# Optimization experiments

Hardware: AMD Instinct MI355X
Metric: run time of the kernel (lower is better)

The kernel has to match this reference:

```python
import jax, jax.numpy as jnp
import numpy as np

N_NODES = 20000
N_EDGES = 320000
EMB = 256
K_DIFF = 3
BN_EPS = 1e-5


def conv1d(x, w, b, stride):
    # x: [N, Cin, L], w: [Cout, Cin, K]
    y = jax.lax.conv_general_dilated(x, w, window_strides=(stride,), padding='VALID',
                                     dimension_numbers=('NCH', 'OIH', 'NCH'))
    return y + b[None, :, None]


def batchnorm_train(x, gamma, beta):
    # training-mode BatchNorm1d over (N, L) per channel, biased variance
    m = jnp.mean(x, axis=(0, 2), keepdims=True)
    v = jnp.var(x, axis=(0, 2), keepdims=True)
    return (x - m) * jax.lax.rsqrt(v + BN_EPS) * gamma[None, :, None] + beta[None, :, None]


def dconv(X, W, b, row, col, norm_out, norm_in, n):
    # Diffusion convolution (pytorch_geometric_temporal DConv), K hops,
    # forward (out-degree) and backward (in-degree) random walks.
    def prop(x, norm):
        msg = norm[:, None] * x[row]                    # [E, F] gather
        return jax.ops.segment_sum(msg, col, num_segments=n)  # scatter-add to targets

    K = W.shape[1]
    Tx_0 = X
    Tx_1 = X
    H = X @ W[0, 0] + X @ W[1, 0]
    if K > 1:
        Tx_1_o = prop(X, norm_out)
        Tx_1_i = prop(X, norm_in)
        H = H + Tx_1_o @ W[0, 1] + Tx_1_i @ W[1, 1]
    for k in range(2, K):
        Tx_2_o = 2.0 * prop(Tx_1_o, norm_out) - Tx_0
        Tx_2_i = 2.0 * prop(Tx_1_i, norm_in) - Tx_0
        H = H + Tx_2_o @ W[0, k] + Tx_2_i @ W[1, k]
        Tx_0, Tx_1_o, Tx_1_i = Tx_1, Tx_2_o, Tx_2_i
    return H + b


def setup_inputs() -> dict:
    key = jax.random.key(0)
    ks = jax.random.split(key, 16)
    d_in = 2 * EMB  # concat([X, H])
    inp = {
        'x': jax.random.normal(ks[0], (N_NODES, 1, 100), dtype=jnp.float32),
        'edge_index': jax.random.randint(ks[1], (2, N_EDGES), 0, N_NODES, dtype=jnp.int32),
        'hidden_state': jax.random.normal(ks[2], (N_NODES, EMB), dtype=jnp.float32),
        'conv1_w': jax.random.normal(ks[3], (32, 1, 10), dtype=jnp.float32) * 0.2,
        'conv1_b': jnp.zeros((32,), jnp.float32),
        'bn1_gamma': jnp.ones((32,), jnp.float32),
        'bn1_beta': jnp.zeros((32,), jnp.float32),
        'conv2_w': jax.random.normal(ks[4], (32, 32, 10), dtype=jnp.float32) * 0.05,
        'conv2_b': jnp.zeros((32,), jnp.float32),
        'bn2_gamma': jnp.ones((32,), jnp.float32),
        'bn2_beta': jnp.zeros((32,), jnp.float32),
        'W_z': jax.random.normal(ks[5], (2, K_DIFF, d_in, EMB), dtype=jnp.float32) * 0.05,
        'b_z': jnp.zeros((EMB,), jnp.float32),
        'W_r': jax.random.normal(ks[6], (2, K_DIFF, d_in, EMB), dtype=jnp.float32) * 0.05,
        'b_r': jnp.zeros((EMB,), jnp.float32),
        'W_h': jax.random.normal(ks[7], (2, K_DIFF, d_in, EMB), dtype=jnp.float32) * 0.05,
        'b_h': jnp.zeros((EMB,), jnp.float32),
    }
    return inp


def reference(x, edge_index, hidden_state, conv1_w, conv1_b, bn1_gamma, bn1_beta,
              conv2_w, conv2_b, bn2_gamma, bn2_beta, W_z, b_z, W_r, b_r, W_h, b_h):
    n = x.shape[0]
    # CNN embedding: conv -> relu -> bn, twice
    h = batchnorm_train(jax.nn.relu(conv1d(x, conv1_w, conv1_b, 3)), bn1_gamma, bn1_beta)
    h = batchnorm_train(jax.nn.relu(conv1d(h, conv2_w, conv2_b, 3)), bn2_gamma, bn2_beta)
    X = h.reshape(n, -1)  # [N, EMB]

    row, col = edge_index[0], edge_index[1]
    ones = jnp.ones((row.shape[0],), X.dtype)
    deg_out = jax.ops.segment_sum(ones, row, num_segments=n)
    deg_in = jax.ops.segment_sum(ones, col, num_segments=n)
    norm_out = (1.0 / deg_out)[row]
    norm_in = (1.0 / deg_in)[col]

    H0 = hidden_state
    XH = jnp.concatenate([X, H0], axis=1)
    Z = jax.nn.sigmoid(dconv(XH, W_z, b_z, row, col, norm_out, norm_in, n))
    R = jax.nn.sigmoid(dconv(XH, W_r, b_r, row, col, norm_out, norm_in, n))
    XRH = jnp.concatenate([X, R * H0], axis=1)
    H_tilde = jnp.tanh(dconv(XRH, W_h, b_h, row, col, norm_out, norm_in, n))
    H = Z * H0 + (1.0 - Z) * H_tilde
    return jax.nn.relu(H)
```

## Files before the change

### kernel.cpp

```cpp
#include <hip/hip_runtime.h>
#include <cstdint>
#include <cstddef>

#define NN 20000
#define NE 320000

typedef float f32x4 __attribute__((ext_vector_type(4)));
typedef short s16x8 __attribute__((ext_vector_type(8)));

struct KB10 { const unsigned short* p[10]; };
struct PPB { const unsigned short* yo0; const unsigned short* yo1;
             const unsigned short* yi0; const unsigned short* yi1;
             unsigned short* po0; unsigned short* po1;
             unsigned short* pi0; unsigned short* pi1; };

__device__ __forceinline__ unsigned short f2bf(float x){
    unsigned u = __float_as_uint(x);
    unsigned r = (u + 0x7fffu + ((u >> 16) & 1u)) >> 16;
    return (unsigned short)r;
}
__device__ __forceinline__ float bf2f(unsigned short s){
    return __uint_as_float(((unsigned)s) << 16);
}

__device__ __forceinline__ void gl16(const void* g, void* l){
    __builtin_amdgcn_global_load_lds((const __attribute__((address_space(1))) unsigned int*)g,
                                     (__attribute__((address_space(3))) unsigned int*)l, 16, 0, 0);
}


__global__ void k_zero(uint32_t* p, int n){
    int i = blockIdx.x*256 + threadIdx.x;
    if(i < n) p[i] = 0u;
}

__global__ void k_degree(const int* __restrict__ ei, int* degout, int* degin){
    int e = blockIdx.x*256 + threadIdx.x;
    if(e < NE){
        atomicAdd(&degout[ei[e]], 1);
        atomicAdd(&degin[ei[NE+e]], 1);
    }
}

__global__ void k_scan(const int* __restrict__ degin, int* __restrict__ coloff,
                       float* __restrict__ invdegin){
    __shared__ int part[1024];
    int t = threadIdx.x;
    int base = t*20;
    int s = 0;
    for(int k=0;k<20;k++){ int i = base+k; if(i < NN) s += degin[i]; }
    part[t] = s;
    __syncthreads();
    for(int off=1; off<1024; off<<=1){
        int v = (t>=off) ? part[t-off] : 0;
        __syncthreads();
        part[t] += v;
        __syncthreads();
    }
    int run = (t>0) ? part[t-1] : 0;
    for(int k=0;k<20;k++){
        int i = base+k;
        if(i < NN){
            int d = degin[i];
            coloff[i] = run;
            run += d;
            invdegin[i] = (d>0) ? (1.0f/(float)d) : 0.0f;
        }
    }
    if(t==1023) coloff[NN] = part[1023];
}

__global__ void k_csr(const int* __restrict__ ei, const int* __restrict__ degout,
                      const int* __restrict__ coloff, int* cnt,
                      int* __restrict__ esrc, float* __restrict__ enormo){
    int e = blockIdx.x*256 + threadIdx.x;
    if(e < NE){
        int r = ei[e], c = ei[NE+e];
        int pos = coloff[c] + atomicAdd(&cnt[c], 1);
        esrc[pos] = r;
        enormo[pos] = 1.0f/(float)degout[r];
    }
}


__global__ void k_conv1(const float* __restrict__ x, const float* __restrict__ w1,
                        const float* __restrict__ b1, unsigned short* __restrict__ y1b){
    __shared__ float w[320];
    __shared__ float bb[32];
    int t = threadIdx.x;
    for(int i=t;i<320;i+=256) w[i] = w1[i];
    if(t < 32) bb[t] = b1[t];
    __syncthreads();
    int gid = blockIdx.x*256 + t;
    if(gid >= NN*31) return;
    int node = gid/31, p = gid - node*31;
    const float* xr = x + node*100 + 3*p;
    float xv[10];
    #pragma unroll
    for(int k=0;k<10;k++) xv[k] = xr[k];
    unsigned short* yo = y1b + (size_t)node*1024 + p;
    #pragma unroll
    for(int c=0;c<32;c++){
        float a = bb[c];
        #pragma unroll
        for(int k=0;k<10;k++) a = fmaf(w[c*10+k], xv[k], a);
        yo[c*32] = f2bf(fmaxf(a, 0.0f));
    }
    if(p == 0){
        #pragma unroll
        for(int c=0;c<32;c++) y1b[(size_t)node*1024 + c*32 + 31] = 0;
    }
}

template<int SLOTS, int PPC>
__global__ void k_chanstats_bf(const unsigned short* __restrict__ y, float* __restrict__ sq){
    int tid = blockIdx.x*blockDim.x + threadIdx.x;
    int slot = tid & (SLOTS-1);
    int node0 = tid / SLOTS;
    int nstride = (gridDim.x*blockDim.x) / SLOTS;
    int c = slot / PPC;
    float s = 0.f, q = 0.f;
    for(int n=node0; n<NN; n+=nstride){
        float v = bf2f(y[(size_t)n*SLOTS + slot]);
        s += v; q = fmaf(v, v, q);
    }
    #pragma unroll
    for(int m=PPC>>1; m>0; m>>=1){
        s += __shfl_xor(s, m);
        q += __shfl_xor(q, m);
    }
    if((threadIdx.x & (PPC-1)) == 0){
        atomicAdd(&sq[c], s);
        atomicAdd(&sq[32+c], q);
    }
}

__global__ void k_bnfin(const float* __restrict__ sq, const float* __restrict__ gamma,
                        const float* __restrict__ beta, float* __restrict__ scsh,
                        float inv_count){
    int c = threadIdx.x;
    if(c < 32){
        float m = sq[c]*inv_count;
        float v = sq[32+c]*inv_count - m*m;
        float sc = gamma[c]*rsqrtf(v + 1e-5f);
        scsh[c] = sc;
        scsh[32+c] = beta[c] - m*sc;
    }
}

__global__ void __launch_bounds__(256) k_conv2(const unsigned short* __restrict__ y1b,
                        const float* __restrict__ w2, const float* __restrict__ b2,
                        const float* __restrict__ scsh1, unsigned short* __restrict__ Xpre){
    __shared__ float wlds[10240];
    __shared__ float hlds[8*1040];
    int t = threadIdx.x;
    int node0 = blockIdx.x*8;
    #pragma unroll
    for(int j=0;j<40;j++){
        int idx = j*256 + t;
        int ck = idx>>5, c2 = idx&31;
        wlds[ck*32 + c2] = w2[c2*320 + ck];
    }
    #pragma unroll
    for(int j=0;j<32;j++){
        int idx = j*256 + t;
        int nl = idx>>10, i = idx&1023;
        int c = i>>5;
        hlds[nl*1040 + i] = fmaf(scsh1[c], bf2f(y1b[(size_t)(node0+nl)*1024 + i]), scsh1[32+c]);
    }
    __syncthreads();
    int nl = t>>5, c2 = t&31;
    int hbase = nl*1040;
    float acc[8];
    float b = b2[c2];
    #pragma unroll
    for(int p=0;p<8;p++) acc[p] = b;
    for(int c=0;c<32;c++){
        float wr[10];
        #pragma unroll
        for(int k=0;k<10;k++) wr[k] = wlds[(c*10+k)*32 + c2];
        float hv[32];
        #pragma unroll
        for(int q=0;q<8;q++){
            float4 v = *(const float4*)&hlds[hbase + c*32 + q*4];
            hv[q*4+0]=v.x; hv[q*4+1]=v.y; hv[q*4+2]=v.z; hv[q*4+3]=v.w;
        }
        #pragma unroll
        for(int p=0;p<8;p++){
            #pragma unroll
            for(int k=0;k<10;k++)
                acc[p] = fmaf(wr[k], hv[3*p+k], acc[p]);
        }
    }
    uint4 pk;
    pk.x = ((unsigned)f2bf(fmaxf(acc[1],0.f))<<16) | f2bf(fmaxf(acc[0],0.f));
    pk.y = ((unsigned)f2bf(fmaxf(acc[3],0.f))<<16) | f2bf(fmaxf(acc[2],0.f));
    pk.z = ((unsigned)f2bf(fmaxf(acc[5],0.f))<<16) | f2bf(fmaxf(acc[4],0.f));
    pk.w = ((unsigned)f2bf(fmaxf(acc[7],0.f))<<16) | f2bf(fmaxf(acc[6],0.f));
    *(uint4*)&Xpre[(size_t)(node0+nl)*256 + c2*8] = pk;
}

__global__ void k_bnapply_bf(const unsigned short* __restrict__ Xpre,
                             const float* __restrict__ scsh,
                             unsigned short* __restrict__ Xb){
    int gid = blockIdx.x*256 + threadIdx.x;
    int c = (gid & 255) >> 3;
    Xb[gid] = f2bf(fmaf(scsh[c], bf2f(Xpre[gid]), scsh[32+c]));
}

__global__ void k_tobf16(const float* __restrict__ a, unsigned short* __restrict__ b){
    int gid = blockIdx.x*256 + threadIdx.x;
    b[gid] = f2bf(a[gid]);
}


__device__ __forceinline__ float weff_val(const float* W, int term, size_t base){
    const size_t S = 512*256;
    if(term==0)      return W[0*S+base] + W[3*S+base] - W[2*S+base] - W[5*S+base];
    else if(term==1) return W[1*S+base];
    else if(term==2) return W[4*S+base];
    else if(term==3) return 2.0f*W[2*S+base];
    else             return 2.0f*W[5*S+base];
}

__global__ void k_weff_zr_t(const float* __restrict__ Wz, const float* __restrict__ Wr,
                            unsigned short* __restrict__ Wt){
    int k = blockIdx.x*256 + threadIdx.x;
    int col = blockIdx.y;
    const float* W = (col < 256) ? Wz : Wr;
    int j = col & 255;
    int kb = k >> 8, rr = k & 255;
    size_t base = (size_t)((kb & 1)*256 + rr)*256 + j;
    Wt[(size_t)col*2560 + k] = f2bf(weff_val(W, kb>>1, base));
}

__global__ void k_weff_h_t(const float* __restrict__ Wh, unsigned short* __restrict__ Wt){
    int k = blockIdx.x*256 + threadIdx.x;
    int col = blockIdx.y;
    int kb = k >> 8, rr = k & 255;
    size_t base = (size_t)((kb & 1)*256 + rr)*256 + col;
    Wt[(size_t)col*2560 + k] = f2bf(weff_val(Wh, kb>>1, base));
}


template<int NB, bool SAME>
__device__ __forceinline__ void acc_edge(const unsigned short* const* yo,
        const unsigned short* const* yi, size_t off, float w,
        float (*ao)[4], float (*ai)[4]){
    #pragma unroll
    for(int b=0;b<NB;b++){
        uint2 uo = *(const uint2*)(yo[b] + off);
        float fo0 = __uint_as_float(uo.x << 16), fo1 = __uint_as_float(uo.x & 0xffff0000u);
        float fo2 = __uint_as_float(uo.y << 16), fo3 = __uint_as_float(uo.y & 0xffff0000u);
        float fi0, fi1, fi2, fi3;
        if(SAME){ fi0=fo0; fi1=fo1; fi2=fo2; fi3=fo3; }
        else{
            uint2 ui = *(const uint2*)(yi[b] + off);
            fi0 = __uint_as_float(ui.x << 16); fi1 = __uint_as_float(ui.x & 0xffff0000u);
            fi2 = __uint_as_float(ui.y << 16); fi3 = __uint_as_float(ui.y & 0xffff0000u);
        }
        ao[b][0] = fmaf(w, fo0, ao[b][0]); ao[b][1] = fmaf(w, fo1, ao[b][1]);
        ao[b][2] = fmaf(w, fo2, ao[b][2]); ao[b][3] = fmaf(w, fo3, ao[b][3]);
        ai[b][0] += fi0; ai[b][1] += fi1; ai[b][2] += fi2; ai[b][3] += fi3;
    }
}

template<int NB, bool SAME>
__global__ void __launch_bounds__(256) k_prop(PPB a,
        const int* __restrict__ coloff, const int* __restrict__ esrc,
        const float* __restrict__ enormo, const float* __restrict__ invdegin){
    int node = blockIdx.x*4 + (threadIdx.x>>6);
    if(node >= NN) return;
    int lane = threadIdx.x & 63;
    int s = coloff[node], e = coloff[node+1];
    float ao[NB][4], ai[NB][4];
    #pragma unroll
    for(int b=0;b<NB;b++){
        #pragma unroll
        for(int q=0;q<4;q++){ ao[b][q]=0.f; ai[b][q]=0.f; }
    }
    const unsigned short* yo[2] = {a.yo0, a.yo1};
    const unsigned short* yi[2] = {a.yi0, a.yi1};
    int j = s;
    for(; j+1 < e; j += 2){
        int s0 = esrc[j], s1 = esrc[j+1];
        float w0 = enormo[j], w1 = enormo[j+1];
        size_t off0 = (size_t)s0*256 + lane*4;
        size_t off1 = (size_t)s1*256 + lane*4;
        acc_edge<NB,SAME>(yo, yi, off0, w0, ao, ai);
        acc_edge<NB,SAME>(yo, yi, off1, w1, ao, ai);
    }
    if(j < e){
        size_t off = (size_t)esrc[j]*256 + lane*4;
        acc_edge<NB,SAME>(yo, yi, off, enormo[j], ao, ai);
    }
    float wi = invdegin[node];
    unsigned short* po[2] = {a.po0, a.po1};
    unsigned short* pi[2] = {a.pi0, a.pi1};
    size_t oo = (size_t)node*256 + lane*4;
    #pragma unroll
    for(int b=0;b<NB;b++){
        uint2 o, q;
        o.x = ((unsigned)f2bf(ao[b][1])<<16) | f2bf(ao[b][0]);
        o.y = ((unsigned)f2bf(ao[b][3])<<16) | f2bf(ao[b][2]);
        q.x = ((unsigned)f2bf(wi*ai[b][1])<<16) | f2bf(wi*ai[b][0]);
        q.y = ((unsigned)f2bf(wi*ai[b][3])<<16) | f2bf(wi*ai[b][2]);
        *(uint2*)(po[b] + oo) = o;
        *(uint2*)(pi[b] + oo) = q;
    }
}


template<int MODE>
__global__ void __launch_bounds__(256) k_gemm(KB10 blocks, const unsigned short* __restrict__ Wt,
        const float* __restrict__ bias0, const float* __restrict__ bias1,
        const float* __restrict__ h0, const float* __restrict__ Zin,
        float* __restrict__ out0, unsigned short* __restrict__ out1){
    __shared__ unsigned short As[4096];
    __shared__ unsigned short Bs[4096];
    int t = threadIdx.x;
    int wid = t >> 6, lane = t & 63;
    int l15 = lane & 15, kg = lane >> 4;
    int row0 = blockIdx.y * 128;
    int col0 = blockIdx.x * 128;
    int rowbase = (wid >> 1) * 64, colbase = (wid & 1) * 64;
    int swz = (l15 >> 1) & 3;
    f32x4 acc[4][4] = {};

    int c0 = t, c1 = t + 256;
    int sr0 = c0 >> 2, sg0 = (c0 & 3) ^ ((sr0 >> 1) & 3);
    int sr1 = c1 >> 2, sg1 = (c1 & 3) ^ ((sr1 >> 1) & 3);
    int gra0 = row0 + sr0; gra0 = (gra0 < NN) ? gra0 : NN-1;
    int gra1 = row0 + sr1; gra1 = (gra1 < NN) ? gra1 : NN-1;

    for(int kb=0; kb<10; kb++){
        const unsigned short* Ap = blocks.p[kb];
        const unsigned short* Wp = Wt + (size_t)kb*256;
        for(int kt=0; kt<256; kt+=32){
            gl16(Ap + (size_t)gra0*256 + kt + sg0*8, As + c0*8);
            gl16(Ap + (size_t)gra1*256 + kt + sg1*8, As + c1*8);
            gl16(Wp + (size_t)(col0+sr0)*2560 + kt + sg0*8, Bs + c0*8);
            gl16(Wp + (size_t)(col0+sr1)*2560 + kt + sg1*8, Bs + c1*8);
            __syncthreads();
            s16x8 af[4], bf[4];
            #pragma unroll
            for(int i=0;i<4;i++){
                int row = rowbase + i*16 + l15;
                af[i] = *(const s16x8*)&As[(row*4 + (kg ^ swz))*8];
                int col = colbase + i*16 + l15;
                bf[i] = *(const s16x8*)&Bs[(col*4 + (kg ^ swz))*8];
            }
            #pragma unroll
            for(int mi=0;mi<4;mi++){
                #pragma unroll
                for(int ni=0;ni<4;ni++){
                    acc[mi][ni] = __builtin_amdgcn_mfma_f32_16x16x32_bf16(
                        af[mi], bf[ni], acc[mi][ni], 0, 0, 0);
                }
            }
            __syncthreads();
        }
    }

    #pragma unroll
    for(int mi=0;mi<4;mi++){
        int gr0 = row0 + rowbase + mi*16 + kg*4;
        #pragma unroll
        for(int ni=0;ni<4;ni++){
            int j = col0 + colbase + ni*16 + l15;
            #pragma unroll
            for(int r=0;r<4;r++){
                int gr = gr0 + r;
                if(gr < NN){
                    float a = acc[mi][ni][r];
                    if(MODE == 0){
                        if(j < 256){
                            out0[(size_t)gr*256 + j] = 1.0f/(1.0f + expf(-(a + bias0[j])));
                        }else{
                            int jj = j - 256;
                            float rv = 1.0f/(1.0f + expf(-(a + bias1[jj])));
                            out1[(size_t)gr*256 + jj] = f2bf(rv * h0[(size_t)gr*256 + jj]);
                        }
                    }else{
                        float z = Zin[(size_t)gr*256 + j];
                        float ht = tanhf(a + bias0[j]);
                        float H = z*h0[(size_t)gr*256 + j] + (1.0f - z)*ht;
                        out0[(size_t)gr*256 + j] = fmaxf(H, 0.0f);
                    }
                }
            }
        }
    }
}


extern "C" void kernel_launch(void* const* d_in, const int* in_sizes, int n_in,
                              void* d_out, int out_size, void* d_ws, size_t ws_size,
                              hipStream_t stream){
    const float* x   = (const float*)d_in[0];
    const int*   ei  = (const int*)  d_in[1];
    const float* h0  = (const float*)d_in[2];
    const float* w1  = (const float*)d_in[3];
    const float* b1  = (const float*)d_in[4];
    const float* g1  = (const float*)d_in[5];
    const float* be1 = (const float*)d_in[6];
    const float* w2  = (const float*)d_in[7];
    const float* b2  = (const float*)d_in[8];
    const float* g2  = (const float*)d_in[9];
    const float* be2 = (const float*)d_in[10];
    const float* Wz  = (const float*)d_in[11];
    const float* bz  = (const float*)d_in[12];
    const float* Wr  = (const float*)d_in[13];
    const float* br  = (const float*)d_in[14];
    const float* Wh  = (const float*)d_in[15];
    const float* bh  = (const float*)d_in[16];
    float* out = (float*)d_out;
    float* wsf = (float*)d_ws;
    (void)in_sizes; (void)n_in; (void)out_size;

    const size_t O_DEGO=0, O_DEGI=20000, O_CNT=40000, O_BN=60000;
    const size_t O_COLOFF=60288, O_ESRC=80384, O_ENORMO=400384, O_INVDEG=720384;
    const size_t O_WTZR=740480, O_WTH=1395840;
    const size_t O_XF=1723520;
    const size_t O_XB=6843520, O_H0B=9403520;
    const size_t O_T1OX=11963520, O_T1IX=14523520, O_P2OX=17083520, O_P2IX=19643520;
    const size_t O_HS0=22203520, O_HS1=24763520, O_HS2=27323520, O_HS3=29883520;
    const size_t O_RH=32443520, O_Z=35003520;
    const size_t WS_NEED_BYTES = (size_t)40123520 * 4;
    if(ws_size < WS_NEED_BYTES) return;

    int* degout = (int*)(wsf + O_DEGO);
    int* degin  = (int*)(wsf + O_DEGI);
    int* cnt    = (int*)(wsf + O_CNT);
    float* bn   = wsf + O_BN;
    int* coloff = (int*)(wsf + O_COLOFF);
    int* esrc   = (int*)(wsf + O_ESRC);
    float* enormo = wsf + O_ENORMO;
    float* invdeg = wsf + O_INVDEG;
    unsigned short* Wtzr = (unsigned short*)(wsf + O_WTZR);
    unsigned short* Wth  = (unsigned short*)(wsf + O_WTH);
    unsigned short* Xpre = (unsigned short*)(wsf + O_XF);
    unsigned short* Xb   = (unsigned short*)(wsf + O_XB);
    unsigned short* h0b  = (unsigned short*)(wsf + O_H0B);
    unsigned short* T1oX = (unsigned short*)(wsf + O_T1OX);
    unsigned short* T1iX = (unsigned short*)(wsf + O_T1IX);
    unsigned short* P2oX = (unsigned short*)(wsf + O_P2OX);
    unsigned short* P2iX = (unsigned short*)(wsf + O_P2IX);
    unsigned short* HS0  = (unsigned short*)(wsf + O_HS0);
    unsigned short* HS1  = (unsigned short*)(wsf + O_HS1);
    unsigned short* HS2  = (unsigned short*)(wsf + O_HS2);
    unsigned short* HS3  = (unsigned short*)(wsf + O_HS3);
    unsigned short* RH   = (unsigned short*)(wsf + O_RH);
    float* Z = wsf + O_Z;
    unsigned short* y1b = (unsigned short*)(wsf + O_T1OX);

    k_zero<<<236,256,0,stream>>>((uint32_t*)(wsf + O_DEGO), 60256);
    k_degree<<<1250,256,0,stream>>>(ei, degout, degin);
    k_scan<<<1,1024,0,stream>>>(degin, coloff, invdeg);
    k_csr<<<1250,256,0,stream>>>(ei, degout, coloff, cnt, esrc, enormo);

    k_conv1<<<2422,256,0,stream>>>(x, w1, b1, y1b);
    k_chanstats_bf<1024,32><<<256,256,0,stream>>>(y1b, bn+0);
    k_bnfin<<<1,32,0,stream>>>(bn+0, g1, be1, bn+64, 1.0f/620000.0f);
    k_conv2<<<2500,256,0,stream>>>(y1b, w2, b2, bn+64, Xpre);
    k_chanstats_bf<256,8><<<64,256,0,stream>>>(Xpre, bn+128);
    k_bnfin<<<1,32,0,stream>>>(bn+128, g2, be2, bn+192, 1.0f/160000.0f);
    k_bnapply_bf<<<20000,256,0,stream>>>(Xpre, bn+192, Xb);
    k_tobf16<<<20000,256,0,stream>>>(h0, h0b);

    k_weff_zr_t<<<dim3(10,512),256,0,stream>>>(Wz, Wr, Wtzr);
    k_weff_h_t<<<dim3(10,256),256,0,stream>>>(Wh, Wth);

    PPB p1; p1.yo0=Xb; p1.yo1=h0b; p1.yi0=Xb; p1.yi1=h0b;
    p1.po0=T1oX; p1.po1=HS0; p1.pi0=T1iX; p1.pi1=HS1;
    k_prop<2,true><<<5000,256,0,stream>>>(p1, coloff, esrc, enormo, invdeg);

    PPB p2; p2.yo0=T1oX; p2.yo1=HS0; p2.yi0=T1iX; p2.yi1=HS1;
    p2.po0=P2oX; p2.po1=HS2; p2.pi0=P2iX; p2.pi1=HS3;
    k_prop<2,false><<<5000,256,0,stream>>>(p2, coloff, esrc, enormo, invdeg);

    KB10 bzr = {{ Xb, h0b, T1oX, HS0, T1iX, HS1, P2oX, HS2, P2iX, HS3 }};
    k_gemm<0><<<dim3(4,157),256,0,stream>>>(bzr, Wtzr, bz, br, h0, nullptr, Z, RH);

    PPB q1; q1.yo0=RH; q1.yo1=nullptr; q1.yi0=RH; q1.yi1=nullptr;
    q1.po0=HS0; q1.po1=nullptr; q1.pi0=HS1; q1.pi1=nullptr;
    k_prop<1,true><<<5000,256,0,stream>>>(q1, coloff, esrc, enormo, invdeg);
    PPB q2; q2.yo0=HS0; q2.yo1=nullptr; q2.yi0=HS1; q2.yi1=nullptr;
    q2.po0=HS2; q2.po1=nullptr; q2.pi0=HS3; q2.pi1=nullptr;
    k_prop<1,false><<<5000,256,0,stream>>>(q2, coloff, esrc, enormo, invdeg);

    KB10 bhh = {{ Xb, RH, T1oX, HS0, T1iX, HS1, P2oX, HS2, P2iX, HS3 }};
    k_gemm<1><<<dim3(2,157),256,0,stream>>>(bhh, Wth, bh, nullptr, h0, Z, out, nullptr);
}
```

Measured before the change: 797.9 us.

## Retile GEMM with K64 and XCD-aware block mapping, batch prop loads, fuse prep

```diff
diff --git a/kernel.cpp b/kernel.cpp
--- a/kernel.cpp
+++ b/kernel.cpp
@@ -200,17 +200,13 @@
     *(uint4*)&Xpre[(size_t)(node0+nl)*256 + c2*8] = pk;
 }
 
-__global__ void k_bnapply_bf(const unsigned short* __restrict__ Xpre,
-                             const float* __restrict__ scsh,
-                             unsigned short* __restrict__ Xb){
+__global__ void k_prep(const unsigned short* __restrict__ Xpre, const float* __restrict__ scsh,
+                       const float* __restrict__ h0, unsigned short* __restrict__ Xb,
+                       unsigned short* __restrict__ h0b){
     int gid = blockIdx.x*256 + threadIdx.x;
     int c = (gid & 255) >> 3;
     Xb[gid] = f2bf(fmaf(scsh[c], bf2f(Xpre[gid]), scsh[32+c]));
-}
-
-__global__ void k_tobf16(const float* __restrict__ a, unsigned short* __restrict__ b){
-    int gid = blockIdx.x*256 + threadIdx.x;
-    b[gid] = f2bf(a[gid]);
+    h0b[gid] = f2bf(h0[gid]);
 }
 
 
@@ -243,26 +239,21 @@
 }
 
 
-template<int NB, bool SAME>
-__device__ __forceinline__ void acc_edge(const unsigned short* const* yo,
-        const unsigned short* const* yi, size_t off, float w,
-        float (*ao)[4], float (*ai)[4]){
-    #pragma unroll
-    for(int b=0;b<NB;b++){
-        uint2 uo = *(const uint2*)(yo[b] + off);
-        float fo0 = __uint_as_float(uo.x << 16), fo1 = __uint_as_float(uo.x & 0xffff0000u);
-        float fo2 = __uint_as_float(uo.y << 16), fo3 = __uint_as_float(uo.y & 0xffff0000u);
-        float fi0, fi1, fi2, fi3;
-        if(SAME){ fi0=fo0; fi1=fo1; fi2=fo2; fi3=fo3; }
-        else{
-            uint2 ui = *(const uint2*)(yi[b] + off);
-            fi0 = __uint_as_float(ui.x << 16); fi1 = __uint_as_float(ui.x & 0xffff0000u);
-            fi2 = __uint_as_float(ui.y << 16); fi3 = __uint_as_float(ui.y & 0xffff0000u);
-        }
-        ao[b][0] = fmaf(w, fo0, ao[b][0]); ao[b][1] = fmaf(w, fo1, ao[b][1]);
-        ao[b][2] = fmaf(w, fo2, ao[b][2]); ao[b][3] = fmaf(w, fo3, ao[b][3]);
-        ai[b][0] += fi0; ai[b][1] += fi1; ai[b][2] += fi2; ai[b][3] += fi3;
-    }
+__device__ __forceinline__ void upd(uint2 u, float w, float* ao4, float* ai4){
+    float f0 = __uint_as_float(u.x << 16), f1 = __uint_as_float(u.x & 0xffff0000u);
+    float f2 = __uint_as_float(u.y << 16), f3 = __uint_as_float(u.y & 0xffff0000u);
+    ao4[0] = fmaf(w, f0, ao4[0]); ao4[1] = fmaf(w, f1, ao4[1]);
+    ao4[2] = fmaf(w, f2, ao4[2]); ao4[3] = fmaf(w, f3, ao4[3]);
+    ai4[0] += f0; ai4[1] += f1; ai4[2] += f2; ai4[3] += f3;
+}
+__device__ __forceinline__ void upd2(uint2 uo, uint2 ui, float w, float* ao4, float* ai4){
+    float o0 = __uint_as_float(uo.x << 16), o1 = __uint_as_float(uo.x & 0xffff0000u);
+    float o2 = __uint_as_float(uo.y << 16), o3 = __uint_as_float(uo.y & 0xffff0000u);
+    float i0 = __uint_as_float(ui.x << 16), i1 = __uint_as_float(ui.x & 0xffff0000u);
+    float i2 = __uint_as_float(ui.y << 16), i3 = __uint_as_float(ui.y & 0xffff0000u);
+    ao4[0] = fmaf(w, o0, ao4[0]); ao4[1] = fmaf(w, o1, ao4[1]);
+    ao4[2] = fmaf(w, o2, ao4[2]); ao4[3] = fmaf(w, o3, ao4[3]);
+    ai4[0] += i0; ai4[1] += i1; ai4[2] += i2; ai4[3] += i3;
 }
 
 template<int NB, bool SAME>
@@ -282,17 +273,49 @@
     const unsigned short* yo[2] = {a.yo0, a.yo1};
     const unsigned short* yi[2] = {a.yi0, a.yi1};
     int j = s;
-    for(; j+1 < e; j += 2){
-        int s0 = esrc[j], s1 = esrc[j+1];
-        float w0 = enormo[j], w1 = enormo[j+1];
-        size_t off0 = (size_t)s0*256 + lane*4;
-        size_t off1 = (size_t)s1*256 + lane*4;
-        acc_edge<NB,SAME>(yo, yi, off0, w0, ao, ai);
-        acc_edge<NB,SAME>(yo, yi, off1, w1, ao, ai);
-    }
-    if(j < e){
+    for(; j+3 < e; j += 4){
+        int e0=esrc[j], e1=esrc[j+1], e2=esrc[j+2], e3=esrc[j+3];
+        float w0=enormo[j], w1=enormo[j+1], w2=enormo[j+2], w3=enormo[j+3];
+        size_t o0=(size_t)e0*256+lane*4, o1=(size_t)e1*256+lane*4;
+        size_t o2=(size_t)e2*256+lane*4, o3=(size_t)e3*256+lane*4;
+        uint2 A0[NB], A1[NB], A2[NB], A3[NB];
+        #pragma unroll
+        for(int b=0;b<NB;b++){
+            A0[b]=*(const uint2*)(yo[b]+o0); A1[b]=*(const uint2*)(yo[b]+o1);
+            A2[b]=*(const uint2*)(yo[b]+o2); A3[b]=*(const uint2*)(yo[b]+o3);
+        }
+        if(SAME){
+            #pragma unroll
+            for(int b=0;b<NB;b++){
+                upd(A0[b], w0, ao[b], ai[b]); upd(A1[b], w1, ao[b], ai[b]);
+                upd(A2[b], w2, ao[b], ai[b]); upd(A3[b], w3, ao[b], ai[b]);
+            }
+        }else{
+            uint2 B0[NB], B1[NB], B2[NB], B3[NB];
+            #pragma unroll
+            for(int b=0;b<NB;b++){
+                B0[b]=*(const uint2*)(yi[b]+o0); B1[b]=*(const uint2*)(yi[b]+o1);
+                B2[b]=*(const uint2*)(yi[b]+o2); B3[b]=*(const uint2*)(yi[b]+o3);
+            }
+            #pragma unroll
+            for(int b=0;b<NB;b++){
+                upd2(A0[b], B0[b], w0, ao[b], ai[b]); upd2(A1[b], B1[b], w1, ao[b], ai[b]);
+                upd2(A2[b], B2[b], w2, ao[b], ai[b]); upd2(A3[b], B3[b], w3, ao[b], ai[b]);
+            }
+        }
+    }
+    for(; j < e; j++){
         size_t off = (size_t)esrc[j]*256 + lane*4;
-        acc_edge<NB,SAME>(yo, yi, off, enormo[j], ao, ai);
+        float w = enormo[j];
+        #pragma unroll
+        for(int b=0;b<NB;b++){
+            uint2 uo = *(const uint2*)(yo[b] + off);
+            if(SAME) upd(uo, w, ao[b], ai[b]);
+            else{
+                uint2 ui = *(const uint2*)(yi[b] + off);
+                upd2(uo, ui, w, ao[b], ai[b]);
+            }
+        }
     }
     float wi = invdegin[node];
     unsigned short* po[2] = {a.po0, a.po1};
@@ -311,51 +334,69 @@
 }
 
 
-template<int MODE>
+template<int MODE, int BNT>
 __global__ void __launch_bounds__(256) k_gemm(KB10 blocks, const unsigned short* __restrict__ Wt,
         const float* __restrict__ bias0, const float* __restrict__ bias1,
         const float* __restrict__ h0, const float* __restrict__ Zin,
         float* __restrict__ out0, unsigned short* __restrict__ out1){
-    __shared__ unsigned short As[4096];
-    __shared__ unsigned short Bs[4096];
+    constexpr int WN = BNT/32;
+    constexpr int NBCH = BNT*8/256;
+    __shared__ unsigned short As[128*64];
+    __shared__ unsigned short Bs[BNT*64];
     int t = threadIdx.x;
     int wid = t >> 6, lane = t & 63;
     int l15 = lane & 15, kg = lane >> 4;
-    int row0 = blockIdx.y * 128;
-    int col0 = blockIdx.x * 128;
-    int rowbase = (wid >> 1) * 64, colbase = (wid & 1) * 64;
-    int swz = (l15 >> 1) & 3;
-    f32x4 acc[4][4] = {};
-
-    int c0 = t, c1 = t + 256;
-    int sr0 = c0 >> 2, sg0 = (c0 & 3) ^ ((sr0 >> 1) & 3);
-    int sr1 = c1 >> 2, sg1 = (c1 & 3) ^ ((sr1 >> 1) & 3);
-    int gra0 = row0 + sr0; gra0 = (gra0 < NN) ? gra0 : NN-1;
-    int gra1 = row0 + sr1; gra1 = (gra1 < NN) ? gra1 : NN-1;
+
+    int bid = blockIdx.x;
+    int xcd = bid & 7, sblk = bid >> 3;
+    int cidx = sblk & 3, r = (sblk >> 2)*8 + xcd;
+    if(r >= 157) return;
+    int row0 = r*128, col0 = cidx*BNT;
+    int rowbase = (wid >> 1)*64, colbase = (wid & 1)*(BNT/2);
+
+    int rcA[4], sgA[4], graA[4];
+    #pragma unroll
+    for(int i=0;i<4;i++){
+        int c = t + i*256;
+        rcA[i] = c >> 3;
+        sgA[i] = (c & 7) ^ (rcA[i] & 7);
+        int gr = row0 + rcA[i];
+        graA[i] = (gr < NN) ? gr : NN-1;
+    }
+
+    f32x4 acc[4][WN] = {};
 
     for(int kb=0; kb<10; kb++){
         const unsigned short* Ap = blocks.p[kb];
         const unsigned short* Wp = Wt + (size_t)kb*256;
-        for(int kt=0; kt<256; kt+=32){
-            gl16(Ap + (size_t)gra0*256 + kt + sg0*8, As + c0*8);
-            gl16(Ap + (size_t)gra1*256 + kt + sg1*8, As + c1*8);
-            gl16(Wp + (size_t)(col0+sr0)*2560 + kt + sg0*8, Bs + c0*8);
-            gl16(Wp + (size_t)(col0+sr1)*2560 + kt + sg1*8, Bs + c1*8);
+        for(int kt=0; kt<256; kt+=64){
+            #pragma unroll
+            for(int i=0;i<4;i++)
+                gl16(Ap + (size_t)graA[i]*256 + kt + sgA[i]*8, As + (t+i*256)*8);
+            #pragma unroll
+            for(int i=0;i<NBCH;i++)
+                gl16(Wp + (size_t)(col0+rcA[i])*2560 + kt + sgA[i]*8, Bs + (t+i*256)*8);
             __syncthreads();
-            s16x8 af[4], bf[4];
-            #pragma unroll
-            for(int i=0;i<4;i++){
-                int row = rowbase + i*16 + l15;
-                af[i] = *(const s16x8*)&As[(row*4 + (kg ^ swz))*8];
-                int col = colbase + i*16 + l15;
-                bf[i] = *(const s16x8*)&Bs[(col*4 + (kg ^ swz))*8];
-            }
-            #pragma unroll
-            for(int mi=0;mi<4;mi++){
+            #pragma unroll
+            for(int ks=0;ks<2;ks++){
+                s16x8 af[4], bfr[WN];
                 #pragma unroll
-                for(int ni=0;ni<4;ni++){
-                    acc[mi][ni] = __builtin_amdgcn_mfma_f32_16x16x32_bf16(
-                        af[mi], bf[ni], acc[mi][ni], 0, 0, 0);
+                for(int i=0;i<4;i++){
+                    int row = rowbase + i*16 + l15;
+                    af[i] = *(const s16x8*)&As[(row*8 + ((ks*4+kg) ^ (row&7)))*8];
+                }
+                #pragma unroll
+                for(int n=0;n<WN;n++){
+                    int colr = colbase + n*16 + l15;
+                    bfr[n] = *(const s16x8*)&Bs[(colr*8 + ((ks*4+kg) ^ (colr&7)))*8];
+                }
+                #pragma unroll
+                for(int mi=0;mi<4;mi++){
+                    #pragma unroll
+                    for(int ni=0;ni<WN;ni++){
+                        acc[mi][ni] = __builtin_amdgcn_mfma_f32_16x16x32_bf16(
+                            af[mi], bfr[ni], acc[mi][ni], 0, 0, 0);
+                    }
                 }
             }
             __syncthreads();
@@ -366,13 +407,13 @@
     for(int mi=0;mi<4;mi++){
         int gr0 = row0 + rowbase + mi*16 + kg*4;
         #pragma unroll
-        for(int ni=0;ni<4;ni++){
+        for(int ni=0;ni<WN;ni++){
             int j = col0 + colbase + ni*16 + l15;
             #pragma unroll
-            for(int r=0;r<4;r++){
-                int gr = gr0 + r;
+            for(int rr=0;rr<4;rr++){
+                int gr = gr0 + rr;
                 if(gr < NN){
-                    float a = acc[mi][ni][r];
+                    float a = acc[mi][ni][rr];
                     if(MODE == 0){
                         if(j < 256){
                             out0[(size_t)gr*256 + j] = 1.0f/(1.0f + expf(-(a + bias0[j])));
@@ -465,8 +506,7 @@
     k_conv2<<<2500,256,0,stream>>>(y1b, w2, b2, bn+64, Xpre);
     k_chanstats_bf<256,8><<<64,256,0,stream>>>(Xpre, bn+128);
     k_bnfin<<<1,32,0,stream>>>(bn+128, g2, be2, bn+192, 1.0f/160000.0f);
-    k_bnapply_bf<<<20000,256,0,stream>>>(Xpre, bn+192, Xb);
-    k_tobf16<<<20000,256,0,stream>>>(h0, h0b);
+    k_prep<<<20000,256,0,stream>>>(Xpre, bn+192, h0, Xb, h0b);
 
     k_weff_zr_t<<<dim3(10,512),256,0,stream>>>(Wz, Wr, Wtzr);
     k_weff_h_t<<<dim3(10,256),256,0,stream>>>(Wh, Wth);
@@ -480,7 +520,7 @@
     k_prop<2,false><<<5000,256,0,stream>>>(p2, coloff, esrc, enormo, invdeg);
 
     KB10 bzr = {{ Xb, h0b, T1oX, HS0, T1iX, HS1, P2oX, HS2, P2iX, HS3 }};
-    k_gemm<0><<<dim3(4,157),256,0,stream>>>(bzr, Wtzr, bz, br, h0, nullptr, Z, RH);
+    k_gemm<0,128><<<640,256,0,stream>>>(bzr, Wtzr, bz, br, h0, nullptr, Z, RH);
 
     PPB q1; q1.yo0=RH; q1.yo1=nullptr; q1.yi0=RH; q1.yi1=nullptr;
     q1.po0=HS0; q1.po1=nullptr; q1.pi0=HS1; q1.pi1=nullptr;
@@ -490,5 +530,5 @@
     k_prop<1,false><<<5000,256,0,stream>>>(q2, coloff, esrc, enormo, invdeg);
 
     KB10 bhh = {{ Xb, RH, T1oX, HS0, T1iX, HS1, P2oX, HS2, P2iX, HS3 }};
-    k_gemm<1><<<dim3(2,157),256,0,stream>>>(bhh, Wth, bh, nullptr, h0, Z, out, nullptr);
-}
+    k_gemm<1,64><<<640,256,0,stream>>>(bhh, Wth, bh, nullptr, h0, Z, out, nullptr);
+}
```

Measured after the change: 769.6 us. 3.6% less time.
